# Kernel optimization log

Measured on AMD Instinct MI355X. Metric: run time of the kernel, lower is better.

The kernel has to match this reference:

```python
import jax, jax.numpy as jnp
import numpy as np

N_NEG = 60
TEMP = 0.07

def _normalize(x, axis):
    n = jnp.sqrt(jnp.sum(x * x, axis=axis, keepdims=True))
    return x / jnp.maximum(n, 1e-12)

def _grid_sample(img, grid):
    # img [B,C,H,W], grid [B,h,w,2] in [-1,1]; bilinear, padding_mode='border', align_corners=False
    B, C, H, W = img.shape
    ix = jnp.clip((grid[..., 0] + 1.0) * (W * 0.5) - 0.5, 0.0, W - 1.0)
    iy = jnp.clip((grid[..., 1] + 1.0) * (H * 0.5) - 0.5, 0.0, H - 1.0)
    x0 = jnp.floor(ix); y0 = jnp.floor(iy)
    x1 = jnp.minimum(x0 + 1.0, W - 1.0); y1 = jnp.minimum(y0 + 1.0, H - 1.0)
    wx = (ix - x0)[:, None]; wy = (iy - y0)[:, None]  # [B,1,h,w]
    imgf = img.reshape(B, C, H * W)
    hh, ww = grid.shape[1], grid.shape[2]
    def gat(yy, xx):
        idx = (yy * W + xx).astype(jnp.int32).reshape(B, 1, hh * ww)
        return jnp.take_along_axis(imgf, idx, axis=2).reshape(B, C, hh, ww)
    v00 = gat(y0, x0); v01 = gat(y0, x1); v10 = gat(y1, x0); v11 = gat(y1, x1)
    return (v00 * (1 - wx) * (1 - wy) + v01 * wx * (1 - wy)
            + v10 * (1 - wx) * wy + v11 * wx * wy)

def _forward(ref_fms, tgt_fms, target_l, target_r, queue):
    b, c, h, w = ref_fms.shape
    s = target_l.shape[-1] // w  # integer downscale factor (nearest interpolate == strided slice)
    disps_l = target_l[:, :, ::s, ::s] / float(s)   # [b,1,h,w]
    disps_r = target_r[:, :, ::s, ::s] / float(s)
    xb = jnp.broadcast_to(jnp.linspace(0.0, 1.0, w), (b, h, w))
    yb = jnp.broadcast_to(jnp.linspace(0.0, 1.0, h)[:, None], (b, h, w))

    def warp(img, disp):
        g = jnp.stack([xb + disp[:, 0] / w, yb], axis=-1)
        return _grid_sample(img, 2.0 * g - 1.0)

    # occlusion / validity mask (detached in the original)
    index = jnp.broadcast_to(jnp.arange(w, dtype=ref_fms.dtype), (b, 1, h, w))
    l2r2l = warp(warp(index, disps_r), -disps_l)
    masko = jnp.abs(index - l2r2l)[:, 0] < 3.0
    mask = masko & (disps_l[:, 0] > 0.0) & (xb - disps_l[:, 0] / w >= 0.0)
    mask = jax.lax.stop_gradient(mask).astype(ref_fms.dtype)  # [b,h,w]

    query = _normalize(ref_fms, 1)
    # positive: warp right feature to left view via disparity
    gpos = jnp.stack([xb - disps_l[:, 0] / w, yb], axis=-1)
    positive = _normalize(_grid_sample(tgt_fms, 2.0 * gpos - 1.0), 1)
    l_pos = jnp.einsum('bchw,bchw->bhw', query, positive)[..., None]

    # negatives: random integer pixel shifts around positive location
    # (no n_neg-fold repeat of tgt_fms; vmap grid_sample over the n axis instead)
    k1, k2 = jax.random.split(jax.random.key(1234))
    mag = jax.random.randint(k1, (b, h, w, N_NEG), 1, 25).astype(ref_fms.dtype)
    sgn = jnp.sign(jax.random.uniform(k2, (b, h, w, N_NEG)) - 0.5).astype(ref_fms.dtype)
    x_right = (xb - disps_l[:, 0] / w) * w
    fx = jnp.mod(x_right[..., None] + mag * sgn, float(w)) / w
    fy = fx / h  # faithful to original code (y coord reuses the normalized x coord)
    grids = jnp.moveaxis(jnp.stack([fx, fy], axis=-1), 3, 0)  # [n,b,h,w,2]
    neg = jax.vmap(lambda g: _grid_sample(tgt_fms, 2.0 * g - 1.0))(grids)  # [n,b,c,h,w]
    neg = _normalize(jnp.moveaxis(neg, 0, -1), 1)  # [b,c,h,w,n]
    l_neg = jnp.einsum('bchw,bchwn->bhwn', query, neg)

    qn = _normalize(queue, 0)  # forward re-normalizes the queue each call
    l_q = jnp.einsum('bchw,ck->bhwk', query, jax.lax.stop_gradient(qn))

    logits = jnp.concatenate([l_pos, l_neg, l_q], axis=-1) * mask[..., None]
    logits = logits.reshape(b * h * w, -1) / TEMP
    # CrossEntropyLoss with all-zero labels (positive is class 0)
    return jnp.mean(-jax.nn.log_softmax(logits, axis=-1)[:, 0])

def setup_inputs():
    key = jax.random.key(0)
    k1, k2, k3, k4, k5 = jax.random.split(key, 5)
    b, c, h, w = 2, 128, 64, 128
    H, W = 4 * h, 4 * w
    return {
        'ref_fms': jax.random.normal(k1, (b, c, h, w), jnp.float32),
        'tgt_fms': jax.random.normal(k2, (b, c, h, w), jnp.float32),
        'target_l': jax.random.uniform(k3, (b, 1, H, W), jnp.float32) * 64.0,
        'target_r': jax.random.uniform(k4, (b, 1, H, W), jnp.float32) * 64.0,
        'queue': jax.random.normal(k5, (c, 6000), jnp.float32),
    }

def reference(ref_fms, tgt_fms, target_l, target_r, queue):
    return _forward(ref_fms, tgt_fms, target_l, target_r, queue)
```

## Files before the change

### kernel.cpp

```cpp
#include <hip/hip_runtime.h>
#include <stdint.h>
#include <math.h>

#define HFM 64
#define WFM 128
#define CFM 128
#define BN 2
#define HWFM (HFM*WFM)
#define NPIX (BN*HWFM)
#define KQ 6000
#define KQP 6144
#define NNEG 60
#define NE (NPIX*NNEG)
#define EHALF_U 491520u
#define MSHIFT 15.0f
#define LOG2E 1.4426950408889634f

typedef _Float16 f16_8 __attribute__((ext_vector_type(8)));
typedef _Float16 f16_2 __attribute__((ext_vector_type(2)));
typedef float f32_4 __attribute__((ext_vector_type(4)));

__host__ __device__ __forceinline__ void threefry2x32(uint32_t k0, uint32_t k1,
                                                      uint32_t x0, uint32_t x1,
                                                      uint32_t* o0, uint32_t* o1) {
  uint32_t ks2 = k0 ^ k1 ^ 0x1BD11BDAu;
  x0 += k0; x1 += k1;
#define TFR(r) { x0 += x1; x1 = (x1 << (r)) | (x1 >> (32 - (r))); x1 ^= x0; }
  TFR(13) TFR(15) TFR(26) TFR(6)
  x0 += k1;  x1 += ks2 + 1u;
  TFR(17) TFR(29) TFR(16) TFR(24)
  x0 += ks2; x1 += k0 + 2u;
  TFR(13) TFR(15) TFR(26) TFR(6)
  x0 += k0;  x1 += k1 + 3u;
  TFR(17) TFR(29) TFR(16) TFR(24)
  x0 += k1;  x1 += ks2 + 4u;
  TFR(13) TFR(15) TFR(26) TFR(6)
  x0 += ks2; x1 += k0 + 5u;
#undef TFR
  *o0 = x0; *o1 = x1;
}

__device__ __forceinline__ void gs_coord(float t, float halfdim, float maxc,
                                         int* i0, int* i1, float* w) {
  float g = 2.0f * t - 1.0f;
  float x = (g + 1.0f) * halfdim - 0.5f;
  x = fminf(fmaxf(x, 0.0f), maxc);
  float f = floorf(x);
  *i0 = (int)f;
  *w = x - f;
  *i1 = (int)fminf(f + 1.0f, maxc);
}

__global__ __launch_bounds__(256) void k_A(
    const float* __restrict__ ref, const float* __restrict__ tgt,
    const float* __restrict__ queue,
    const float* __restrict__ target_l, const float* __restrict__ target_r,
    _Float16* __restrict__ refTf, _Float16* __restrict__ tgtTf,
    _Float16* __restrict__ queueTf, float2* __restrict__ qeb,
    float* __restrict__ maskArr, float* __restrict__ xr) {
  __shared__ float tile[64][35];
  int blk = blockIdx.x;
  int tid = threadIdx.x;
  if (blk < 64) {
    int p = blk * 256 + tid;
    int b = p >> 13;
    int rem = p & (HWFM - 1);
    int i = rem >> 7, j = rem & 127;
    const float stepx = 1.0f / 127.0f, stepy = 1.0f / 63.0f;
    float xb = (j == 127) ? 1.0f : j * stepx;
    float yb = (i == 63) ? 1.0f : i * stepy;
    const float* tl = target_l + (size_t)b * 256 * 512;
    const float* tr = target_r + (size_t)b * 256 * 512;
    float dl = tl[(4 * i) * 512 + 4 * j] * 0.25f;
    int y0i, y1i; float wy;
    gs_coord(yb, 32.0f, 63.0f, &y0i, &y1i, &wy);
    float t = xb - dl * (1.0f / 128.0f);
    int x0i, x1i; float wx;
    gs_coord(t, 64.0f, 127.0f, &x0i, &x1i, &wx);
    auto innerv = [&](int y, int x) -> float {
      float xbx = (x == 127) ? 1.0f : x * stepx;
      float drv = tr[(4 * y) * 512 + 4 * x] * 0.25f;
      float ti = xbx + drv * (1.0f / 128.0f);
      float g = 2.0f * ti - 1.0f;
      float ix2 = fminf(fmaxf((g + 1.0f) * 64.0f - 0.5f, 0.0f), 127.0f);
      float x0f = floorf(ix2);
      float wxp = ix2 - x0f;
      float x1f = fminf(x0f + 1.0f, 127.0f);
      return x0f * (1.0f - wxp) + x1f * wxp;
    };
    float v00 = innerv(y0i, x0i), v01 = innerv(y0i, x1i);
    float v10 = innerv(y1i, x0i), v11 = innerv(y1i, x1i);
    float l2r2l = v00 * (1.0f - wx) * (1.0f - wy) + v01 * wx * (1.0f - wy)
                + v10 * (1.0f - wx) * wy + v11 * wx * wy;
    bool masko = fabsf((float)j - l2r2l) < 3.0f;
    bool mk = masko && (dl > 0.0f) && (t >= 0.0f);
    maskArr[p] = mk ? 1.0f : 0.0f;
    xr[p] = t * 128.0f;
  } else if (blk < 88) {
    int k = (blk - 64) * 256 + tid;
    if (k < KQP) {
      if (k >= KQ) { qeb[k] = make_float2(0.0f, -1000.0f); }
      else {
        float ss = 0.0f;
        for (int c = 0; c < CFM; c++) { float v = queue[c * KQ + k]; ss += v * v; }
        float qi = 1.0f / fmaxf(sqrtf(ss), 1e-12f);
        qeb[k] = make_float2(qi * (LOG2E / 0.07f), -MSHIFT * LOG2E);
      }
    }
  } else if (blk < 472) {
    int q = blk - 88;
    int cy = q / 192, nx = q - cy * 192;
    int n0 = nx * 32, c0 = cy * 64;
    int c = tid >> 2, qq = tid & 3;
    const float* sp = queue + (size_t)(c0 + c) * KQ + n0 + qq * 4;
    if (n0 + 32 <= KQ) {
      float4 v0 = *(const float4*)sp;
      float4 v1 = *(const float4*)(sp + 16);
      tile[c][qq * 4 + 0] = v0.x; tile[c][qq * 4 + 1] = v0.y;
      tile[c][qq * 4 + 2] = v0.z; tile[c][qq * 4 + 3] = v0.w;
      tile[c][qq * 4 + 16] = v1.x; tile[c][qq * 4 + 17] = v1.y;
      tile[c][qq * 4 + 18] = v1.z; tile[c][qq * 4 + 19] = v1.w;
    } else {
#pragma unroll
      for (int k = 0; k < 4; k++) {
        int n = n0 + qq * 4 + k;
        tile[c][qq * 4 + k] = (n < KQ) ? sp[k] : 0.0f;
        tile[c][qq * 4 + 16 + k] = (n + 16 < KQ) ? sp[16 + k] : 0.0f;
      }
    }
    __syncthreads();
    int x = tid >> 3, j8 = tid & 7;
    f16_8 o;
#pragma unroll
    for (int k = 0; k < 8; k++) o[k] = (_Float16)tile[j8 * 8 + k][x];
    *(f16_8*)(queueTf + (size_t)(n0 + x) * CFM + c0 + j8 * 8) = o;
  } else {
    int fblk = blk - 472;
    int z = fblk >> 9, rem2 = fblk & 511;
    int cy = rem2 >> 8, xt = rem2 & 255;
    int x0 = xt * 32, c0 = cy * 64;
    int arr = z >> 1, b = z & 1;
    const float* src = (arr == 0 ? ref : tgt) + (size_t)b * CFM * HWFM;
    _Float16* dst = (arr == 0 ? refTf : tgtTf) + (size_t)b * HWFM * CFM;
    int c = tid >> 2, qq = tid & 3;
    const float* sp = src + (size_t)(c0 + c) * HWFM + x0 + qq * 4;
    float4 v0 = *(const float4*)sp;
    float4 v1 = *(const float4*)(sp + 16);
    tile[c][qq * 4 + 0] = v0.x; tile[c][qq * 4 + 1] = v0.y;
    tile[c][qq * 4 + 2] = v0.z; tile[c][qq * 4 + 3] = v0.w;
    tile[c][qq * 4 + 16] = v1.x; tile[c][qq * 4 + 17] = v1.y;
    tile[c][qq * 4 + 18] = v1.z; tile[c][qq * 4 + 19] = v1.w;
    __syncthreads();
    int x = tid >> 3, j8 = tid & 7;
    f16_8 o;
#pragma unroll
    for (int k = 0; k < 8; k++) o[k] = (_Float16)tile[j8 * 8 + k][x];
    *(f16_8*)(dst + (size_t)(x0 + x) * CFM + c0 + j8 * 8) = o;
  }
}

__global__ __launch_bounds__(256) void k_B(
    const _Float16* __restrict__ refTf, const _Float16* __restrict__ tgtTf,
    _Float16* __restrict__ QTf, float* __restrict__ stats,
    const float* __restrict__ maskArr, const float* __restrict__ xr,
    float* __restrict__ S, float* __restrict__ logit0,
    int* __restrict__ count, int* __restrict__ list) {
  __shared__ int wsum[4];
  int blk = blockIdx.x;
  int tid = threadIdx.x;
  int lane = tid & 63;
  if (blk == 0) {
    int wave = tid >> 6;
    int base_p = tid * 64;
    unsigned long long bits = 0ull;
    const float4* m4 = (const float4*)(maskArr + base_p);
#pragma unroll
    for (int k = 0; k < 16; k++) {
      float4 v = m4[k];
      if (v.x > 0.0f) bits |= 1ull << (4 * k + 0);
      if (v.y > 0.0f) bits |= 1ull << (4 * k + 1);
      if (v.z > 0.0f) bits |= 1ull << (4 * k + 2);
      if (v.w > 0.0f) bits |= 1ull << (4 * k + 3);
    }
    int m = __popcll(bits);
    int scan = m;
#pragma unroll
    for (int off = 1; off < 64; off <<= 1) {
      int n = __shfl_up(scan, off, 64);
      if (lane >= off) scan += n;
    }
    if (lane == 63) wsum[wave] = scan;
    __syncthreads();
    int wbase = 0;
    for (int w = 0; w < wave; w++) wbase += wsum[w];
    int idx = wbase + scan - m;
    for (int k = 0; k < 64; k++) {
      if ((bits >> k) & 1ull) list[idx++] = base_p + k;
    }
    if (tid == 255) *count = idx;
  } else if (blk < 65) {
    int sub = tid >> 6;
    int xg = (blk - 1) * 4 + sub;
    int b = xg >> 7, x = xg & 127;
    int xp = min(x + 1, 127);
    int c2 = lane * 2;
    int base = b * HWFM;
    f16_2 c0  = *(const f16_2*)(tgtTf + (size_t)(base + x) * CFM + c2);
    f16_2 c1  = *(const f16_2*)(tgtTf + (size_t)(base + WFM + x) * CFM + c2);
    f16_2 c0p = *(const f16_2*)(tgtTf + (size_t)(base + xp) * CFM + c2);
    f16_2 c1p = *(const f16_2*)(tgtTf + (size_t)(base + WFM + xp) * CFM + c2);
    float a0 = (float)c0[0], a1 = (float)c0[1];
    float b0 = (float)c1[0], b1 = (float)c1[1];
    float p0 = (float)c0p[0], p1 = (float)c0p[1];
    float q0 = (float)c1p[0], q1 = (float)c1p[1];
    float s[7];
    s[0] = a0 * a0 + a1 * a1;
    s[1] = a0 * b0 + a1 * b1;
    s[2] = b0 * b0 + b1 * b1;
    s[3] = a0 * p0 + a1 * p1;
    s[4] = a0 * q0 + a1 * q1;
    s[5] = b0 * p0 + b1 * p1;
    s[6] = b0 * q0 + b1 * q1;
#pragma unroll
    for (int o = 32; o; o >>= 1)
#pragma unroll
      for (int k = 0; k < 7; k++) s[k] += __shfl_xor(s[k], o, 64);
    if (lane == 0) {
      float* st = stats + (size_t)xg * 8;
#pragma unroll
      for (int k = 0; k < 7; k++) st[k] = s[k];
      st[7] = 0.0f;
    }
  } else {
    int wave = tid >> 6;
    int p = (blk - 65) * 4 + wave;
    float mk = maskArr[p];
    if (mk == 0.0f) return;
    int b = p >> 13;
    int rem = p & (HWFM - 1);
    int i = rem >> 7;
    const float stepy = 1.0f / 63.0f;
    float yb = (i == 63) ? 1.0f : i * stepy;
    float t = xr[p] * (1.0f / 128.0f);
    int y0i, y1i; float wy;
    gs_coord(yb, 32.0f, 63.0f, &y0i, &y1i, &wy);
    int x0i, x1i; float wx;
    gs_coord(t, 64.0f, 127.0f, &x0i, &x1i, &wx);

    int c2 = lane * 2;
    f16_2 q2 = *(const f16_2*)(refTf + (size_t)p * CFM + c2);
    int bo = b * HWFM;
    f16_2 a2 = *(const f16_2*)(tgtTf + (size_t)(bo + y0i * WFM + x0i) * CFM + c2);
    f16_2 b2 = *(const f16_2*)(tgtTf + (size_t)(bo + y0i * WFM + x1i) * CFM + c2);
    f16_2 cc2 = *(const f16_2*)(tgtTf + (size_t)(bo + y1i * WFM + x0i) * CFM + c2);
    f16_2 d2 = *(const f16_2*)(tgtTf + (size_t)(bo + y1i * WFM + x1i) * CFM + c2);

    float w00 = (1.0f - wx) * (1.0f - wy), w01 = wx * (1.0f - wy);
    float w10 = (1.0f - wx) * wy,          w11 = wx * wy;
    float q0 = (float)q2[0], q1 = (float)q2[1];
    float v0 = w00 * (float)a2[0] + w01 * (float)b2[0] + w10 * (float)cc2[0] + w11 * (float)d2[0];
    float v1 = w00 * (float)a2[1] + w01 * (float)b2[1] + w10 * (float)cc2[1] + w11 * (float)d2[1];

    float s0 = q0 * q0 + q1 * q1;
    float s1 = q0 * v0 + q1 * v1;
    float s2 = v0 * v0 + v1 * v1;
#pragma unroll
    for (int o = 32; o; o >>= 1) {
      s0 += __shfl_xor(s0, o, 64);
      s1 += __shfl_xor(s1, o, 64);
      s2 += __shfl_xor(s2, o, 64);
    }
    float inv = 1.0f / fmaxf(sqrtf(s0), 1e-12f);
    f16_2 qw; qw[0] = (_Float16)(q0 * inv); qw[1] = (_Float16)(q1 * inv);
    *(f16_2*)(QTf + (size_t)p * CFM + c2) = qw;
    if (lane == 0) {
      float lpos = (s1 * inv) / fmaxf(sqrtf(s2), 1e-12f);
      float lg0 = lpos / 0.07f;
      logit0[p] = lg0;
      S[p] = expf(lg0 - MSHIFT);
    }
  }
}

__global__ __launch_bounds__(256, 2) void k_gemm(
    const _Float16* __restrict__ QTf,
    const _Float16* __restrict__ queueTf,
    const _Float16* __restrict__ tgtTf,
    const float2* __restrict__ qeb,
    float* __restrict__ S, float* __restrict__ D,
    const int* __restrict__ count, const int* __restrict__ list) {
  __shared__ _Float16 Bs[2][128 * CFM];
  __shared__ float Srow[128];
  __shared__ int pb[128];
  int tid = threadIdx.x;
  int cnt = *count;
  int pblk = blockIdx.y * 128;
  if (pblk >= cnt) return;
  int wave = tid >> 6, lane = tid & 63;
  int quad = lane >> 4, l16 = lane & 15;
  int wm = wave >> 1, wn = wave & 1;

  if (tid < 128) {
    Srow[tid] = 0.0f;
    pb[tid] = list[min(pblk + tid, cnt - 1)] >> 13;
  }

  f16_8 Af[4][4];
  int r0 = pblk + wm * 64;
#pragma unroll
  for (int mt = 0; mt < 4; mt++) {
    int prow = list[min(r0 + mt * 16 + l16, cnt - 1)];
    const _Float16* arow = QTf + (size_t)prow * CFM + quad * 8;
#pragma unroll
    for (int ks = 0; ks < 4; ks++)
      Af[mt][ks] = *(const f16_8*)(arow + ks * 32);
  }

  int lrow = lane >> 4, lchunk = lane & 15;
  auto stage = [&](const _Float16* bsrc, int buf) {
#pragma unroll
    for (int i = 0; i < 8; i++) {
      int rb = wave * 32 + i * 4;
      int r = rb + lrow;
      const _Float16* g = bsrc + (size_t)r * CFM + ((lchunk ^ (r & 7)) << 3);
      __builtin_amdgcn_global_load_lds(
          (const __attribute__((address_space(1))) void*)g,
          (__attribute__((address_space(3))) void*)(&Bs[buf][rb * CFM]),
          16, 0, 0);
    }
  };

  int nbase = blockIdx.x * 8 * 128;
  int cur;
  float rowsum[4][4] = {{0,0,0,0},{0,0,0,0},{0,0,0,0},{0,0,0,0}};

  if (blockIdx.x < 4) {
    int batch = blockIdx.x >> 1;
    stage(tgtTf + ((size_t)batch * HWFM + (blockIdx.x & 1) * 128) * CFM, 0);
    __syncthreads();
    stage(queueTf + (size_t)nbase * CFM, 1);
    f32_4 acc[4][4];
#pragma unroll
    for (int mt = 0; mt < 4; mt++)
#pragma unroll
      for (int nt = 0; nt < 4; nt++)
        acc[mt][nt] = (f32_4){0.0f, 0.0f, 0.0f, 0.0f};
#pragma unroll
    for (int ks = 0; ks < 4; ks++) {
      f16_8 Bk[4];
#pragma unroll
      for (int nt = 0; nt < 4; nt++) {
        int brow = wn * 64 + nt * 16 + l16;
        Bk[nt] = *(const f16_8*)(&Bs[0][brow * CFM + ((ks * 32 + quad * 8) ^ ((brow & 7) * 8))]);
      }
#pragma unroll
      for (int mt = 0; mt < 4; mt++)
#pragma unroll
        for (int nt = 0; nt < 4; nt++)
          acc[mt][nt] = __builtin_amdgcn_mfma_f32_16x16x32_f16(Af[mt][ks], Bk[nt], acc[mt][nt], 0, 0, 0);
    }
#pragma unroll
    for (int mt = 0; mt < 4; mt++)
#pragma unroll
      for (int nt = 0; nt < 4; nt++)
#pragma unroll
        for (int r = 0; r < 4; r++) {
          int rowloc = wm * 64 + mt * 16 + quad * 4 + r;
          int slot = pblk + rowloc;
          int colL = (blockIdx.x & 1) * 128 + wn * 64 + nt * 16 + l16;
          if (slot < cnt && pb[rowloc] == batch)
            D[(size_t)slot * 256 + colL] = acc[mt][nt][r];
        }
    __syncthreads();
    cur = 1;
  } else {
    stage(queueTf + (size_t)nbase * CFM, 0);
    __syncthreads();
    cur = 0;
  }

#pragma unroll
  for (int ic = 0; ic < 8; ic++) {
    int n0 = nbase + ic * 128;
    if (ic + 1 < 8) stage(queueTf + (size_t)(n0 + 128) * CFM, cur ^ 1);
    float2 qb[4];
#pragma unroll
    for (int nt = 0; nt < 4; nt++) qb[nt] = qeb[n0 + wn * 64 + nt * 16 + l16];

    f32_4 acc[4][4];
#pragma unroll
    for (int mt = 0; mt < 4; mt++)
#pragma unroll
      for (int nt = 0; nt < 4; nt++)
        acc[mt][nt] = (f32_4){0.0f, 0.0f, 0.0f, 0.0f};
#pragma unroll
    for (int ks = 0; ks < 4; ks++) {
      f16_8 Bk[4];
#pragma unroll
      for (int nt = 0; nt < 4; nt++) {
        int brow = wn * 64 + nt * 16 + l16;
        Bk[nt] = *(const f16_8*)(&Bs[cur][brow * CFM + ((ks * 32 + quad * 8) ^ ((brow & 7) * 8))]);
      }
#pragma unroll
      for (int mt = 0; mt < 4; mt++)
#pragma unroll
        for (int nt = 0; nt < 4; nt++)
          acc[mt][nt] = __builtin_amdgcn_mfma_f32_16x16x32_f16(Af[mt][ks], Bk[nt], acc[mt][nt], 0, 0, 0);
    }

#pragma unroll
    for (int nt = 0; nt < 4; nt++)
#pragma unroll
      for (int mt = 0; mt < 4; mt++)
#pragma unroll
        for (int r = 0; r < 4; r++)
          rowsum[mt][r] += exp2f(fmaf(acc[mt][nt][r], qb[nt].x, qb[nt].y));
    __syncthreads();
    cur ^= 1;
  }

#pragma unroll
  for (int mt = 0; mt < 4; mt++)
#pragma unroll
    for (int r = 0; r < 4; r++) {
      float vv = rowsum[mt][r];
      vv += __shfl_xor(vv, 1);
      vv += __shfl_xor(vv, 2);
      vv += __shfl_xor(vv, 4);
      vv += __shfl_xor(vv, 8);
      rowsum[mt][r] = vv;
    }
  if (l16 == 0) {
#pragma unroll
    for (int mt = 0; mt < 4; mt++)
#pragma unroll
      for (int r = 0; r < 4; r++)
        atomicAdd(&Srow[wm * 64 + mt * 16 + quad * 4 + r], rowsum[mt][r]);
  }
  __syncthreads();
  if (tid < 128) {
    int pr = pblk + tid;
    if (pr < cnt) atomicAdd(&S[list[pr]], Srow[tid]);
  }
}

__global__ __launch_bounds__(256) void k_negatives_lite(
    const float* __restrict__ D, const float* __restrict__ stats,
    const float* __restrict__ xr, float* __restrict__ S,
    const int* __restrict__ count, const int* __restrict__ list,
    uint32_t k1a, uint32_t k1b, uint32_t k2a, uint32_t k2b) {
  int tid = threadIdx.x;
  int wave = tid >> 6, lane = tid & 63;
  int cnt = *count;
  int slot = blockIdx.x * 4 + wave;
  if (slot >= cnt) return;
  int p = list[slot];
  int b = p >> 13;
  float esum = 0.0f;
  if (lane < NNEG) {
    uint32_t e = (uint32_t)(p * NNEG + lane);
    uint32_t h0, h1;
    threefry2x32(k1a, k1b, e, e + (uint32_t)NE, &h0, &h1);
    uint32_t off = ((h0 % 24u) * 16u + (h1 % 24u)) % 24u;
    float mag = (float)(1u + off);
    uint32_t ub;
    {
      uint32_t a, bm;
      if (e < EHALF_U) { threefry2x32(k2a, k2b, e, e + EHALF_U, &a, &bm); ub = a; }
      else             { threefry2x32(k2a, k2b, e - EHALF_U, e, &a, &bm); ub = bm; }
    }
    float u = __uint_as_float((ub >> 9) | 0x3F800000u) - 1.0f;
    float sg = (u > 0.5f) ? 1.0f : ((u < 0.5f) ? -1.0f : 0.0f);

    float v = xr[p] + mag * sg;
    float r = fmodf(v, 128.0f);
    if (r < 0.0f) r += 128.0f;
    float fx = r * (1.0f / 128.0f);
    float fy = fx * (1.0f / 64.0f);
    int x0i, x1i, y0i, y1i; float wx, wy;
    gs_coord(fx, 64.0f, 127.0f, &x0i, &x1i, &wx);
    gs_coord(fy, 32.0f, 63.0f, &y0i, &y1i, &wy);

    const float* Dp = D + (size_t)slot * 256;
    float d00 = Dp[x0i], d01 = Dp[x1i];
    float d10 = Dp[128 + x0i], d11 = Dp[128 + x1i];
    float u0 = 1.0f - wy, u1 = wy;
    float dv0 = u0 * d00 + u1 * d10;
    float dv1 = u0 * d01 + u1 * d11;
    float dot = (1.0f - wx) * dv0 + wx * dv1;

    const float* st0 = stats + (size_t)(b * 128 + x0i) * 8;
    const float* st1 = stats + (size_t)(b * 128 + x1i) * 8;
    float4 sa = *(const float4*)st0;
    float4 sb = *(const float4*)(st0 + 4);
    float4 sc = *(const float4*)st1;
    float a0 = u0 * u0, a1 = u0 * u1, a2 = u1 * u1;
    float nB0 = a0 * sa.x + 2.0f * a1 * sa.y + a2 * sa.z;
    float nB1 = a0 * sc.x + 2.0f * a1 * sc.y + a2 * sc.z;
    float cB  = a0 * sa.w + a1 * (sb.x + sb.y) + a2 * sb.z;
    float wx0 = 1.0f - wx;
    float nsq = wx0 * wx0 * nB0 + 2.0f * wx * wx0 * cB + wx * wx * nB1;
    float ln = dot / fmaxf(sqrtf(fmaxf(nsq, 0.0f)), 1e-12f);
    esum = __expf(ln * (1.0f / 0.07f) - MSHIFT);
  }
#pragma unroll
  for (int o = 32; o; o >>= 1) esum += __shfl_xor(esum, o, 64);
  if (lane == 0) atomicAdd(&S[p], esum);
}

__global__ __launch_bounds__(1024) void k_finalize(
    const float* __restrict__ S, const float* __restrict__ logit0,
    const float* __restrict__ maskArr, float* __restrict__ out) {
  int tid = threadIdx.x;
  const float cmask = logf(6061.0f);
  double acc = 0.0;
  for (int p = tid; p < NPIX; p += 1024) {
    float term = (maskArr[p] > 0.0f) ? (logf(S[p]) + MSHIFT - logit0[p]) : cmask;
    acc += (double)term;
  }
#pragma unroll
  for (int off = 32; off; off >>= 1) acc += __shfl_down(acc, off, 64);
  __shared__ double sd[16];
  if ((tid & 63) == 0) sd[tid >> 6] = acc;
  __syncthreads();
  if (tid == 0) {
    double tot = 0.0;
    for (int w = 0; w < 16; w++) tot += sd[w];
    out[0] = (float)(tot / (double)NPIX);
  }
}

extern "C" void kernel_launch(void* const* d_in, const int* in_sizes, int n_in,
                              void* d_out, int out_size, void* d_ws, size_t ws_size,
                              hipStream_t stream) {
  const float* ref   = (const float*)d_in[0];
  const float* tgt   = (const float*)d_in[1];
  const float* tl    = (const float*)d_in[2];
  const float* tr    = (const float*)d_in[3];
  const float* queue = (const float*)d_in[4];
  float* out = (float*)d_out;
  float* ws = (float*)d_ws;

  float2* qeb = (float2*)ws;
  float* S    = ws + 12288;
  float* lg0  = ws + 28672;
  float* mk   = ws + 45056;
  float* xr   = ws + 61440;
  int* count  = (int*)(ws + 77824);
  int* list   = (int*)(ws + 77840);
  _Float16* QTf     = (_Float16*)(ws + 94464);
  _Float16* queueTf = (_Float16*)(ws + 1143040);
  _Float16* tgtTf   = (_Float16*)(ws + 1536256);
  _Float16* refTf   = (_Float16*)(ws + 2584832);
  float* stats = ws + 3633408;
  float* D     = ws + 3635456;

  uint32_t b0o0, b0o1, b1o0, b1o1;
  threefry2x32(0u, 1234u, 0u, 2u, &b0o0, &b0o1);
  threefry2x32(0u, 1234u, 1u, 3u, &b1o0, &b1o1);
  uint32_t k1a = b0o0, k1b = b1o0, k2a = b0o1, k2b = b1o1;

  k_A<<<dim3(2520), dim3(256), 0, stream>>>(ref, tgt, queue, tl, tr,
                                            refTf, tgtTf, queueTf, qeb, mk, xr);
  k_B<<<dim3(65 + 4096), dim3(256), 0, stream>>>(refTf, tgtTf, QTf, stats,
                                                 mk, xr, S, lg0, count, list);
  k_gemm<<<dim3(6, NPIX / 128), dim3(256), 0, stream>>>(QTf, queueTf, tgtTf, qeb,
                                                        S, D, count, list);
  k_negatives_lite<<<dim3(NPIX / 4), dim3(256), 0, stream>>>(D, stats, xr, S, count, list,
                                                             k1a, k1b, k2a, k2b);
  k_finalize<<<dim3(1), dim3(1024), 0, stream>>>(S, lg0, mk, out);
}
```

Measured before the change: 135.7 us.

## Restructure queue GEMM into independent per-wave 32-row tiles reading B directly from global

Replaces the 128x128 block tile with LDS double-buffered queue staging by a per-wave decomposition. Each wave owns 32 rows and a 256-column group and loads B fragments straight from global memory into registers, with no LDS and no __syncthreads. The tgt-feature D computation becomes separate wave groups. This is meant to raise parallelism and occupancy and remove barrier stalls. In exchange it loses the LDS reuse of B across waves, adds global/L2 traffic, and issues per-row atomics directly to S.

```diff
diff --git a/kernel.cpp b/kernel.cpp
--- a/kernel.cpp
+++ b/kernel.cpp
@@ -282,165 +282,130 @@
   }
 }
 
-__global__ __launch_bounds__(256, 2) void k_gemm(
+__global__ __launch_bounds__(256) void k_gemm(
     const _Float16* __restrict__ QTf,
     const _Float16* __restrict__ queueTf,
     const _Float16* __restrict__ tgtTf,
     const float2* __restrict__ qeb,
     float* __restrict__ S, float* __restrict__ D,
     const int* __restrict__ count, const int* __restrict__ list) {
-  __shared__ _Float16 Bs[2][128 * CFM];
-  __shared__ float Srow[128];
-  __shared__ int pb[128];
   int tid = threadIdx.x;
-  int cnt = *count;
-  int pblk = blockIdx.y * 128;
-  if (pblk >= cnt) return;
   int wave = tid >> 6, lane = tid & 63;
   int quad = lane >> 4, l16 = lane & 15;
-  int wm = wave >> 1, wn = wave & 1;
-
-  if (tid < 128) {
-    Srow[tid] = 0.0f;
-    pb[tid] = list[min(pblk + tid, cnt - 1)] >> 13;
-  }
-
-  f16_8 Af[4][4];
-  int r0 = pblk + wm * 64;
-#pragma unroll
-  for (int mt = 0; mt < 4; mt++) {
-    int prow = list[min(r0 + mt * 16 + l16, cnt - 1)];
+  int cnt = *count;
+  int gw = blockIdx.x * 4 + wave;
+  int grp = gw >> 9;
+  int rowblk = gw & 511;
+  int slot0 = rowblk * 32;
+  if (slot0 >= cnt) return;
+
+  f16_8 Af[2][4];
+#pragma unroll
+  for (int mt = 0; mt < 2; mt++) {
+    int prow = list[min(slot0 + mt * 16 + l16, cnt - 1)];
     const _Float16* arow = QTf + (size_t)prow * CFM + quad * 8;
 #pragma unroll
     for (int ks = 0; ks < 4; ks++)
       Af[mt][ks] = *(const f16_8*)(arow + ks * 32);
   }
 
-  int lrow = lane >> 4, lchunk = lane & 15;
-  auto stage = [&](const _Float16* bsrc, int buf) {
-#pragma unroll
-    for (int i = 0; i < 8; i++) {
-      int rb = wave * 32 + i * 4;
-      int r = rb + lrow;
-      const _Float16* g = bsrc + (size_t)r * CFM + ((lchunk ^ (r & 7)) << 3);
-      __builtin_amdgcn_global_load_lds(
-          (const __attribute__((address_space(1))) void*)g,
-          (__attribute__((address_space(3))) void*)(&Bs[buf][rb * CFM]),
-          16, 0, 0);
-    }
-  };
-
-  int nbase = blockIdx.x * 8 * 128;
-  int cur;
-  float rowsum[4][4] = {{0,0,0,0},{0,0,0,0},{0,0,0,0},{0,0,0,0}};
-
-  if (blockIdx.x < 4) {
-    int batch = blockIdx.x >> 1;
-    stage(tgtTf + ((size_t)batch * HWFM + (blockIdx.x & 1) * 128) * CFM, 0);
-    __syncthreads();
-    stage(queueTf + (size_t)nbase * CFM, 1);
-    f32_4 acc[4][4];
-#pragma unroll
-    for (int mt = 0; mt < 4; mt++)
+  if (grp < 24) {
+    int n0 = grp * 256;
+    float rowsum[2][4] = {{0.0f,0.0f,0.0f,0.0f},{0.0f,0.0f,0.0f,0.0f}};
+#pragma unroll
+    for (int sub = 0; sub < 4; sub++) {
+      int c0 = n0 + sub * 64;
+      float2 qb[4];
+#pragma unroll
+      for (int nt = 0; nt < 4; nt++) qb[nt] = qeb[c0 + nt * 16 + l16];
+      f32_4 acc[2][4];
+#pragma unroll
+      for (int mt = 0; mt < 2; mt++)
+#pragma unroll
+        for (int nt = 0; nt < 4; nt++)
+          acc[mt][nt] = (f32_4){0.0f, 0.0f, 0.0f, 0.0f};
+#pragma unroll
+      for (int ks = 0; ks < 4; ks++) {
+        f16_8 Bk[4];
+#pragma unroll
+        for (int nt = 0; nt < 4; nt++)
+          Bk[nt] = *(const f16_8*)(queueTf + (size_t)(c0 + nt * 16 + l16) * CFM + ks * 32 + quad * 8);
+#pragma unroll
+        for (int mt = 0; mt < 2; mt++)
+#pragma unroll
+          for (int nt = 0; nt < 4; nt++)
+            acc[mt][nt] = __builtin_amdgcn_mfma_f32_16x16x32_f16(Af[mt][ks], Bk[nt], acc[mt][nt], 0, 0, 0);
+      }
 #pragma unroll
       for (int nt = 0; nt < 4; nt++)
-        acc[mt][nt] = (f32_4){0.0f, 0.0f, 0.0f, 0.0f};
-#pragma unroll
-    for (int ks = 0; ks < 4; ks++) {
-      f16_8 Bk[4];
-#pragma unroll
-      for (int nt = 0; nt < 4; nt++) {
-        int brow = wn * 64 + nt * 16 + l16;
-        Bk[nt] = *(const f16_8*)(&Bs[0][brow * CFM + ((ks * 32 + quad * 8) ^ ((brow & 7) * 8))]);
+#pragma unroll
+        for (int mt = 0; mt < 2; mt++)
+#pragma unroll
+          for (int r = 0; r < 4; r++)
+            rowsum[mt][r] += exp2f(fmaf(acc[mt][nt][r], qb[nt].x, qb[nt].y));
+    }
+#pragma unroll
+    for (int mt = 0; mt < 2; mt++)
+#pragma unroll
+      for (int r = 0; r < 4; r++) {
+        float vv = rowsum[mt][r];
+        vv += __shfl_xor(vv, 1);
+        vv += __shfl_xor(vv, 2);
+        vv += __shfl_xor(vv, 4);
+        vv += __shfl_xor(vv, 8);
+        rowsum[mt][r] = vv;
       }
-#pragma unroll
-      for (int mt = 0; mt < 4; mt++)
+    if (l16 == 0) {
+#pragma unroll
+      for (int mt = 0; mt < 2; mt++)
+#pragma unroll
+        for (int r = 0; r < 4; r++) {
+          int sl = slot0 + mt * 16 + quad * 4 + r;
+          if (sl < cnt) atomicAdd(&S[list[sl]], rowsum[mt][r]);
+        }
+    }
+  } else {
+    int d = grp - 24;
+    int batch = d >> 1, half = d & 1;
+    const _Float16* base = tgtTf + ((size_t)batch * HWFM + half * 128) * CFM;
+    int pbrow[2][4];
+#pragma unroll
+    for (int mt = 0; mt < 2; mt++)
+#pragma unroll
+      for (int r = 0; r < 4; r++)
+        pbrow[mt][r] = list[min(slot0 + mt * 16 + quad * 4 + r, cnt - 1)] >> 13;
+#pragma unroll
+    for (int sub = 0; sub < 2; sub++) {
+      f32_4 acc[2][4];
+#pragma unroll
+      for (int mt = 0; mt < 2; mt++)
 #pragma unroll
         for (int nt = 0; nt < 4; nt++)
-          acc[mt][nt] = __builtin_amdgcn_mfma_f32_16x16x32_f16(Af[mt][ks], Bk[nt], acc[mt][nt], 0, 0, 0);
-    }
-#pragma unroll
-    for (int mt = 0; mt < 4; mt++)
-#pragma unroll
-      for (int nt = 0; nt < 4; nt++)
-#pragma unroll
-        for (int r = 0; r < 4; r++) {
-          int rowloc = wm * 64 + mt * 16 + quad * 4 + r;
-          int slot = pblk + rowloc;
-          int colL = (blockIdx.x & 1) * 128 + wn * 64 + nt * 16 + l16;
-          if (slot < cnt && pb[rowloc] == batch)
-            D[(size_t)slot * 256 + colL] = acc[mt][nt][r];
-        }
-    __syncthreads();
-    cur = 1;
-  } else {
-    stage(queueTf + (size_t)nbase * CFM, 0);
-    __syncthreads();
-    cur = 0;
-  }
-
-#pragma unroll
-  for (int ic = 0; ic < 8; ic++) {
-    int n0 = nbase + ic * 128;
-    if (ic + 1 < 8) stage(queueTf + (size_t)(n0 + 128) * CFM, cur ^ 1);
-    float2 qb[4];
-#pragma unroll
-    for (int nt = 0; nt < 4; nt++) qb[nt] = qeb[n0 + wn * 64 + nt * 16 + l16];
-
-    f32_4 acc[4][4];
-#pragma unroll
-    for (int mt = 0; mt < 4; mt++)
-#pragma unroll
-      for (int nt = 0; nt < 4; nt++)
-        acc[mt][nt] = (f32_4){0.0f, 0.0f, 0.0f, 0.0f};
-#pragma unroll
-    for (int ks = 0; ks < 4; ks++) {
-      f16_8 Bk[4];
-#pragma unroll
-      for (int nt = 0; nt < 4; nt++) {
-        int brow = wn * 64 + nt * 16 + l16;
-        Bk[nt] = *(const f16_8*)(&Bs[cur][brow * CFM + ((ks * 32 + quad * 8) ^ ((brow & 7) * 8))]);
+          acc[mt][nt] = (f32_4){0.0f, 0.0f, 0.0f, 0.0f};
+#pragma unroll
+      for (int ks = 0; ks < 4; ks++) {
+        f16_8 Bk[4];
+#pragma unroll
+        for (int nt = 0; nt < 4; nt++)
+          Bk[nt] = *(const f16_8*)(base + (size_t)(sub * 64 + nt * 16 + l16) * CFM + ks * 32 + quad * 8);
+#pragma unroll
+        for (int mt = 0; mt < 2; mt++)
+#pragma unroll
+          for (int nt = 0; nt < 4; nt++)
+            acc[mt][nt] = __builtin_amdgcn_mfma_f32_16x16x32_f16(Af[mt][ks], Bk[nt], acc[mt][nt], 0, 0, 0);
       }
 #pragma unroll
-      for (int mt = 0; mt < 4; mt++)
+      for (int mt = 0; mt < 2; mt++)
 #pragma unroll
         for (int nt = 0; nt < 4; nt++)
-          acc[mt][nt] = __builtin_amdgcn_mfma_f32_16x16x32_f16(Af[mt][ks], Bk[nt], acc[mt][nt], 0, 0, 0);
-    }
-
-#pragma unroll
-    for (int nt = 0; nt < 4; nt++)
-#pragma unroll
-      for (int mt = 0; mt < 4; mt++)
-#pragma unroll
-        for (int r = 0; r < 4; r++)
-          rowsum[mt][r] += exp2f(fmaf(acc[mt][nt][r], qb[nt].x, qb[nt].y));
-    __syncthreads();
-    cur ^= 1;
-  }
-
-#pragma unroll
-  for (int mt = 0; mt < 4; mt++)
-#pragma unroll
-    for (int r = 0; r < 4; r++) {
-      float vv = rowsum[mt][r];
-      vv += __shfl_xor(vv, 1);
-      vv += __shfl_xor(vv, 2);
-      vv += __shfl_xor(vv, 4);
-      vv += __shfl_xor(vv, 8);
-      rowsum[mt][r] = vv;
-    }
-  if (l16 == 0) {
-#pragma unroll
-    for (int mt = 0; mt < 4; mt++)
-#pragma unroll
-      for (int r = 0; r < 4; r++)
-        atomicAdd(&Srow[wm * 64 + mt * 16 + quad * 4 + r], rowsum[mt][r]);
-  }
-  __syncthreads();
-  if (tid < 128) {
-    int pr = pblk + tid;
-    if (pr < cnt) atomicAdd(&S[list[pr]], Srow[tid]);
+#pragma unroll
+          for (int r = 0; r < 4; r++) {
+            int sl = slot0 + mt * 16 + quad * 4 + r;
+            int colL = half * 128 + sub * 64 + nt * 16 + l16;
+            if (sl < cnt && pbrow[mt][r] == batch)
+              D[(size_t)sl * 256 + colL] = acc[mt][nt][r];
+          }
+    }
   }
 }
 
@@ -564,8 +529,8 @@
                                             refTf, tgtTf, queueTf, qeb, mk, xr);
   k_B<<<dim3(65 + 4096), dim3(256), 0, stream>>>(refTf, tgtTf, QTf, stats,
                                                  mk, xr, S, lg0, count, list);
-  k_gemm<<<dim3(6, NPIX / 128), dim3(256), 0, stream>>>(QTf, queueTf, tgtTf, qeb,
-                                                        S, D, count, list);
+  k_gemm<<<dim3(3584), dim3(256), 0, stream>>>(QTf, queueTf, tgtTf, qeb,
+                                               S, D, count, list);
   k_negatives_lite<<<dim3(NPIX / 4), dim3(256), 0, stream>>>(D, stats, xr, S, count, list,
                                                              k1a, k1b, k2a, k2b);
   k_finalize<<<dim3(1), dim3(1024), 0, stream>>>(S, lg0, mk, out);
```

Measured after the change: 165.7 us. 22.2% more time.
